# Optimization experiments

Hardware: AMD Instinct MI355X
Metric: run time of the kernel (lower is better)

## Reference

```python
import jax, jax.numpy as jnp
import numpy as np


def _dct2(x):
    """DCT-II over last dim, scipy norm=None scaling (matches the torch rfft trick:
    X_k = 2 * sum_n x_n cos(pi*k*(2n+1)/(2N))). Expressed as one batched matmul."""
    N = x.shape[-1]
    n = jnp.arange(N, dtype=x.dtype)
    k = jnp.arange(N, dtype=x.dtype)
    # D[k, n] = 2*cos(pi*k*(2n+1)/(2N))
    D = 2.0 * jnp.cos((np.pi / (2.0 * N)) * k[:, None] * (2.0 * n[None, :] + 1.0))
    return jnp.einsum('kn,bcn->bck', D, x)


def setup_inputs() -> dict:
    key = jax.random.key(0)
    k0, k1, k2 = jax.random.split(key, 3)
    b, c, l = 32, 512, 1024
    x = jax.random.normal(k0, (b, c, l), dtype=jnp.float32)
    # 1x1 Conv1d weights (kernel_size=1, bias=False) stored as [out, in]
    w1 = jax.random.normal(k1, (2 * c, c), dtype=jnp.float32) / np.float32(np.sqrt(c))
    w2 = jax.random.normal(k2, (c, 2 * c), dtype=jnp.float32) / np.float32(np.sqrt(2 * c))
    ln_w = jnp.ones((l,), dtype=jnp.float32)
    ln_b = jnp.zeros((l,), dtype=jnp.float32)
    return {"x": x, "w1": w1, "w2": w2, "ln_w": ln_w, "ln_b": ln_b}


def reference(x, w1, w2, ln_w, ln_b):
    eps = 1e-6
    freq = _dct2(x)                                   # [b, c, l]
    mu = jnp.mean(freq, axis=-1, keepdims=True)
    var = jnp.var(freq, axis=-1, keepdims=True)       # biased, like nn.LayerNorm
    h = (freq - mu) * jax.lax.rsqrt(var + eps) * ln_w + ln_b
    # fc: Conv1d(c->2c, k=1) -> Dropout(eval: identity) -> ReLU -> Conv1d(2c->c) -> Sigmoid
    h = jax.nn.relu(jnp.einsum('oi,bil->bol', w1, h))  # [b, 2c, l]
    gate = jax.nn.sigmoid(jnp.einsum('oi,bil->bol', w2, h))  # [b, c, l]
    return x * gate
```

## Files before the change

### kernel.cpp

```cpp
#include <hip/hip_runtime.h>
#include <hip/hip_bf16.h>
#include <math.h>

typedef short short8 __attribute__((ext_vector_type(8)));
typedef short short4v __attribute__((ext_vector_type(4)));
typedef float f32x4 __attribute__((ext_vector_type(4)));

__device__ __forceinline__ short f2bf(float f) {
  union { float f; unsigned u; } v; v.f = f;
  unsigned r = v.u + 0x7FFFu + ((v.u >> 16) & 1u);
  return (short)(r >> 16);
}
__device__ __forceinline__ float bf2f(short s) {
  union { unsigned u; float f; } v; v.u = ((unsigned)(unsigned short)s) << 16;
  return v.f;
}

__global__ __launch_bounds__(256) void cast_kernel(const float* __restrict__ in,
                                                   short* __restrict__ out, int n4) {
  int i = blockIdx.x * blockDim.x + threadIdx.x;
  if (i < n4) {
    float4 v = ((const float4*)in)[i];
    short4v o;
    o.x = f2bf(v.x); o.y = f2bf(v.y); o.z = f2bf(v.z); o.w = f2bf(v.w);
    ((short4v*)out)[i] = o;
  }
}

__global__ __launch_bounds__(256) void prep_eo(const float* __restrict__ x,
                                               short* __restrict__ eo) {
  int t = blockIdx.x * 256 + threadIdx.x;
  int bc = t >> 7, n0 = (t & 127) * 4;
  const float* xr = x + (size_t)bc * 1024;
  float4 f = *(const float4*)(xr + n0);
  float4 r = *(const float4*)(xr + 1020 - n0);
  short4v ef, of;
  ef.x = f2bf(f.x + r.w); ef.y = f2bf(f.y + r.z); ef.z = f2bf(f.z + r.y); ef.w = f2bf(f.w + r.x);
  of.x = f2bf(f.x - r.w); of.y = f2bf(f.y - r.z); of.z = f2bf(f.z - r.y); of.w = f2bf(f.w - r.x);
  *(short4v*)&eo[(size_t)bc * 512 + n0] = ef;
  *(short4v*)&eo[8388608 + (size_t)bc * 512 + n0] = of;
}

__global__ __launch_bounds__(256) void build_Deo(short* __restrict__ D) {
  int t = blockIdx.x * 256 + threadIdx.x;
  int parity = t >> 18, rem = t & 262143;
  int k2 = rem >> 9, n = rem & 511;
  const float s = 1.5339807878856412e-03f;
  float arg = (s * (float)(2 * k2 + parity)) * (float)(2 * n + 1);
  D[t] = f2bf(2.0f * cosf(arg));
}

__global__ __launch_bounds__(256) void ln_stats(const float2* __restrict__ partial,
                                                float2* __restrict__ musd) {
  int n = blockIdx.x * 256 + threadIdx.x;
  float S = 0.f, Q = 0.f;
#pragma unroll
  for (int r = 0; r < 8; ++r) {
    float2 p = partial[(size_t)r * 16384 + n];
    S += p.x; Q += p.y;
  }
  float mu  = S * (1.f / 1024.f);
  float var = Q * (1.f / 1024.f) - mu * mu;
  float2 o; o.x = mu; o.y = rsqrtf(var + 1e-6f);
  musd[n] = o;
}

__global__ __launch_bounds__(256) void ln_apply(short* __restrict__ freqT,
                                                const float2* __restrict__ musd,
                                                const float* __restrict__ lnw,
                                                const float* __restrict__ lnb) {
  int t = blockIdx.x * 256 + threadIdx.x;
  int c8 = t & 63;
  int k  = (t >> 6) & 1023;
  int b  = t >> 16;
  size_t idx = ((size_t)b << 19) + (size_t)k * 512 + (size_t)c8 * 8;
  short8 v = *(const short8*)&freqT[idx];
  float w  = lnw[k];
  float bb = lnb[k];
  const float2* ms = &musd[b * 512 + c8 * 8];
  short8 o;
#pragma unroll
  for (int j = 0; j < 8; ++j) {
    float f = bf2f(v[j]);
    float2 m = ms[j];
    o[j] = f2bf((f - m.x) * m.y * w + bb);
  }
  *(short8*)&freqT[idx] = o;
}

template<int EPI>
__global__ __launch_bounds__(256, 2) void gemm128(
    const short* __restrict__ A, const short* __restrict__ B,
    void* __restrict__ Cout, const float* __restrict__ X,
    float2* __restrict__ P, int K, int NT, long strideA, long strideB)
{
  __shared__ short As[2][8192];
  __shared__ short Bs[2][8192];
  const int tid = threadIdx.x;
  const int l   = tid & 63;
  const int w   = tid >> 6;
  const int wm  = w >> 1;
  const int wc  = w & 1;
  const int l7  = l & 7;
  const int lr  = l & 15;
  const int lhi = l >> 4;

  const int nwg = gridDim.x, q = nwg >> 3, orig = blockIdx.x;
  const int wgid = (orig & 7) * q + (orig >> 3);
  int bx, by, bz;
  if (EPI == 0)      { bx = wgid & 3; bz = (wgid >> 2) & 1; by = wgid >> 3; }
  else if (EPI == 1) { by = wgid & 7; bx = (wgid >> 3) & 7; bz = wgid >> 6; }
  else               { bx = wgid & 3; by = (wgid >> 2) & 7; bz = wgid >> 5; }

  const long row0 = (long)bx * 128, col0 = (long)by * 128;
  const short* Ab = A + (size_t)bz * strideA + (size_t)row0 * K;
  const short* Bb = B + (size_t)bz * strideB + (size_t)col0 * K;

  const int rowb  = tid >> 3;
  const int colel = ((tid & 7) ^ ((tid >> 3) & 7)) * 8;
  const int abase = (wm * 64 + lr) * 64;
  const int bbase = (wc * 64 + lr) * 64;
  const int s0 = ((lhi    ) ^ l7) * 8;
  const int s1 = ((lhi + 4) ^ l7) * 8;

  f32x4 acc[4][4];
#pragma unroll
  for (int i = 0; i < 4; ++i)
#pragma unroll
    for (int j = 0; j < 4; ++j) acc[i][j] = (f32x4){0.f, 0.f, 0.f, 0.f};

#define GLL(SRC, DST) __builtin_amdgcn_global_load_lds(                      \
      (const __attribute__((address_space(1))) void*)(SRC),                  \
      (__attribute__((address_space(3))) void*)(DST), 16, 0, 0)

#define STAGE(KT, D) do {                                                    \
    const size_t ko_ = (size_t)(KT) * 64 + colel;                            \
    _Pragma("unroll")                                                        \
    for (int r_ = 0; r_ < 4; ++r_)                                           \
      GLL(Ab + (size_t)(r_ * 32 + rowb) * K + ko_,                           \
          &As[D][(r_ * 32 + rowb) * 64 + (tid & 7) * 8]);                    \
    _Pragma("unroll")                                                        \
    for (int r_ = 0; r_ < 4; ++r_)                                           \
      GLL(Bb + (size_t)(r_ * 32 + rowb) * K + ko_,                           \
          &Bs[D][(r_ * 32 + rowb) * 64 + (tid & 7) * 8]);                    \
  } while (0)

#define LD8(PTR, OFF) (*(const short8*)&(PTR)[OFF])
#define MFMA(AV, BV, C) __builtin_amdgcn_mfma_f32_16x16x32_bf16(AV, BV, C, 0, 0, 0)
#define SBAR __builtin_amdgcn_s_barrier()
#define SCHB __builtin_amdgcn_sched_barrier(0)

#define MFMA16(A0, A1, A2, A3, B0, B1, B2, B3)                               \
    __builtin_amdgcn_s_setprio(1);                                           \
    acc[0][0]=MFMA(A0,B0,acc[0][0]); acc[0][1]=MFMA(A0,B1,acc[0][1]);        \
    acc[0][2]=MFMA(A0,B2,acc[0][2]); acc[0][3]=MFMA(A0,B3,acc[0][3]);        \
    acc[1][0]=MFMA(A1,B0,acc[1][0]); acc[1][1]=MFMA(A1,B1,acc[1][1]);        \
    acc[1][2]=MFMA(A1,B2,acc[1][2]); acc[1][3]=MFMA(A1,B3,acc[1][3]);        \
    acc[2][0]=MFMA(A2,B0,acc[2][0]); acc[2][1]=MFMA(A2,B1,acc[2][1]);        \
    acc[2][2]=MFMA(A2,B2,acc[2][2]); acc[2][3]=MFMA(A2,B3,acc[2][3]);        \
    acc[3][0]=MFMA(A3,B0,acc[3][0]); acc[3][1]=MFMA(A3,B1,acc[3][1]);        \
    acc[3][2]=MFMA(A3,B2,acc[3][2]); acc[3][3]=MFMA(A3,B3,acc[3][3]);        \
    __builtin_amdgcn_s_setprio(0);

  STAGE(0, 0);
  STAGE(1, 1);

  int cur = 0;
  for (int kt = 0; kt < NT; ++kt) {
    if (kt + 1 < NT) { asm volatile("s_waitcnt vmcnt(8)" ::: "memory"); }
    else             { asm volatile("s_waitcnt vmcnt(0)" ::: "memory"); }
    SCHB; SBAR;
    const short* Ad = As[cur];
    const short* Bd = Bs[cur];
    short8 a00, a01, a02, a03, b00, b01, b02, b03;
    short8 a10, a11, a12, a13, b10, b11, b12, b13;
    a00 = LD8(Ad, abase + 0 * 1024 + s0);
    a01 = LD8(Ad, abase + 1 * 1024 + s0);
    a02 = LD8(Ad, abase + 2 * 1024 + s0);
    a03 = LD8(Ad, abase + 3 * 1024 + s0);
    b00 = LD8(Bd, bbase + 0 * 1024 + s0);
    b01 = LD8(Bd, bbase + 1 * 1024 + s0);
    b02 = LD8(Bd, bbase + 2 * 1024 + s0);
    b03 = LD8(Bd, bbase + 3 * 1024 + s0);
    a10 = LD8(Ad, abase + 0 * 1024 + s1);
    a11 = LD8(Ad, abase + 1 * 1024 + s1);
    a12 = LD8(Ad, abase + 2 * 1024 + s1);
    a13 = LD8(Ad, abase + 3 * 1024 + s1);
    b10 = LD8(Bd, bbase + 0 * 1024 + s1);
    b11 = LD8(Bd, bbase + 1 * 1024 + s1);
    b12 = LD8(Bd, bbase + 2 * 1024 + s1);
    b13 = LD8(Bd, bbase + 3 * 1024 + s1);
    SCHB;
    asm volatile("s_waitcnt lgkmcnt(8)" ::: "memory");
    SCHB;
    MFMA16(a00, a01, a02, a03, b00, b01, b02, b03)
    SCHB;
    asm volatile("s_waitcnt lgkmcnt(0)" ::: "memory");
    SCHB; SBAR;
    if (kt + 2 < NT) STAGE(kt + 2, cur);
    SCHB;
    MFMA16(a10, a11, a12, a13, b10, b11, b12, b13)
    SCHB;
    cur ^= 1;
  }

  float sv[4], qv[4];
#pragma unroll
  for (int ni = 0; ni < 4; ++ni) { sv[ni] = 0.f; qv[ni] = 0.f; }

#pragma unroll
  for (int mi = 0; mi < 4; ++mi) {
#pragma unroll
    for (int ni = 0; ni < 4; ++ni) {
#pragma unroll
      for (int j = 0; j < 4; ++j) {
        int r  = (int)row0 + wm * 64 + mi * 16 + lhi * 4 + j;
        int cc = (int)col0 + wc * 64 + ni * 16 + lr;
        float v = acc[mi][ni][j];
        if (EPI == 0) {
          sv[ni] += v; qv[ni] += v * v;
          int rr = r * 2 + bz;
          ((short*)Cout)[((size_t)(cc >> 9) << 19) + (size_t)rr * 512 + (cc & 511)] = f2bf(v);
        } else if (EPI == 1) {
          ((short*)Cout)[(size_t)bz * 1048576 + (size_t)r * 1024 + cc] = f2bf(v > 0.f ? v : 0.f);
        } else {
          size_t idx = (size_t)bz * 524288 + (size_t)r * 1024 + cc;
          float g = 1.f / (1.f + __expf(-v));
          ((float*)Cout)[idx] = X[idx] * g;
        }
      }
    }
  }

  if (EPI == 0) {
    __syncthreads();
    float* redS = (float*)&As[0][0];
    float* redQ = redS + 1024;
    const int contrib = wm * 4 + lhi;
#pragma unroll
    for (int ni = 0; ni < 4; ++ni) {
      int ccl = wc * 64 + ni * 16 + lr;
      redS[ccl * 8 + contrib] = sv[ni];
      redQ[ccl * 8 + contrib] = qv[ni];
    }
    __syncthreads();
    if (tid < 128) {
      float S = 0.f, Q = 0.f;
#pragma unroll
      for (int i = 0; i < 8; ++i) { S += redS[tid * 8 + i]; Q += redQ[tid * 8 + i]; }
      float2 o; o.x = S; o.y = Q;
      P[(size_t)(bz * 4 + bx) * 16384 + col0 + tid] = o;
    }
  }
#undef MFMA16
#undef MFMA
#undef LD8
#undef STAGE
#undef GLL
#undef SBAR
#undef SCHB
}

extern "C" void kernel_launch(void* const* d_in, const int* in_sizes, int n_in,
                              void* d_out, int out_size, void* d_ws, size_t ws_size,
                              hipStream_t stream) {
  const float* x    = (const float*)d_in[0];
  const float* w1   = (const float*)d_in[1];
  const float* w2   = (const float*)d_in[2];
  const float* ln_w = (const float*)d_in[3];
  const float* ln_b = (const float*)d_in[4];
  float* out = (float*)d_out;

  char* ws = (char*)d_ws;
  short* Deo    = (short*)(ws);
  short* w1_bf  = (short*)(ws + 1048576);
  short* w2_bf  = (short*)(ws + 2097152);
  short* freqT  = (short*)(ws + 3145728);
  short* z1t    = (short*)(ws + 36700160);
  short* eo     = z1t;
  float2* part  = (float2*)(ws + 103809024);
  float2* musd  = (float2*)(ws + 104857600);

  prep_eo<<<dim3(8192), dim3(256), 0, stream>>>(x, eo);
  cast_kernel<<<dim3(512), dim3(256), 0, stream>>>(w1, w1_bf, 524288 / 4);
  cast_kernel<<<dim3(512), dim3(256), 0, stream>>>(w2, w2_bf, 524288 / 4);
  build_Deo<<<dim3(2048), dim3(256), 0, stream>>>(Deo);

  gemm128<0><<<dim3(1024), dim3(256), 0, stream>>>(
      Deo, eo, (void*)freqT, nullptr, part, 512, 8, 262144, 8388608);

  ln_stats<<<dim3(64), dim3(256), 0, stream>>>(part, musd);

  ln_apply<<<dim3(8192), dim3(256), 0, stream>>>(freqT, musd, ln_w, ln_b);

  gemm128<1><<<dim3(2048), dim3(256), 0, stream>>>(
      freqT, w1_bf, (void*)z1t, nullptr, nullptr, 512, 8, 524288, 0);

  gemm128<2><<<dim3(1024), dim3(256), 0, stream>>>(
      w2_bf, z1t, (void*)out, x, nullptr, 1024, 16, 0, 1048576);
}
```

Measured before the change: 160.5 us.

## Fuse LayerNorm apply into first FC GEMM via operand prologue and epilogue

Removes the separate ln_apply pass over freqT and instead normalizes the A operand (subtract mean, scale by rstd) in registers while staging it into LDS inside a new gemm2ln kernel. The per-k ln weight and bias are applied in the epilogue, using precomputed row sums of w1 computed during the w1 cast. This saves a full read-modify-write of the bf16 frequency tensor and one kernel launch. In exchange, A loads now go through registers instead of direct-to-LDS loads, which adds VALU work and register pressure inside the GEMM main loop.

```diff
diff --git a/kernel.cpp b/kernel.cpp
--- a/kernel.cpp
+++ b/kernel.cpp
@@ -14,6 +14,11 @@
 __device__ __forceinline__ float bf2f(short s) {
   union { unsigned u; float f; } v; v.u = ((unsigned)(unsigned short)s) << 16;
   return v.f;
+}
+__device__ __forceinline__ unsigned cvtpk(float lo, float hi) {
+  unsigned r;
+  asm("v_cvt_pk_bf16_f32 %0, %1, %2" : "=v"(r) : "v"(lo), "v"(hi));
+  return r;
 }
 
 __global__ __launch_bounds__(256) void cast_kernel(const float* __restrict__ in,
@@ -24,6 +29,30 @@
     short4v o;
     o.x = f2bf(v.x); o.y = f2bf(v.y); o.z = f2bf(v.z); o.w = f2bf(v.w);
     ((short4v*)out)[i] = o;
+  }
+}
+
+__global__ __launch_bounds__(256) void w1_prep(const float* __restrict__ w1,
+                                               short* __restrict__ w1_bf,
+                                               float* __restrict__ w1s) {
+  int t = blockIdx.x * 256 + threadIdx.x;
+  int o = t >> 2, qt = t & 3;
+  const float* src = w1 + (size_t)o * 512 + qt * 128;
+  short* dst = w1_bf + (size_t)o * 512 + qt * 128;
+  float s = 0.f;
+#pragma unroll
+  for (int i = 0; i < 128; i += 4) {
+    float4 v = *(const float4*)(src + i);
+    s += v.x + v.y + v.z + v.w;
+    short4v ov; ov.x = f2bf(v.x); ov.y = f2bf(v.y); ov.z = f2bf(v.z); ov.w = f2bf(v.w);
+    *(short4v*)(dst + i) = ov;
+  }
+  __shared__ float red[256];
+  red[threadIdx.x] = s;
+  __syncthreads();
+  if (qt == 0) {
+    int tx = threadIdx.x;
+    w1s[o] = red[tx] + red[tx + 1] + red[tx + 2] + red[tx + 3];
   }
 }
 
@@ -63,29 +92,6 @@
   float var = Q * (1.f / 1024.f) - mu * mu;
   float2 o; o.x = mu; o.y = rsqrtf(var + 1e-6f);
   musd[n] = o;
-}
-
-__global__ __launch_bounds__(256) void ln_apply(short* __restrict__ freqT,
-                                                const float2* __restrict__ musd,
-                                                const float* __restrict__ lnw,
-                                                const float* __restrict__ lnb) {
-  int t = blockIdx.x * 256 + threadIdx.x;
-  int c8 = t & 63;
-  int k  = (t >> 6) & 1023;
-  int b  = t >> 16;
-  size_t idx = ((size_t)b << 19) + (size_t)k * 512 + (size_t)c8 * 8;
-  short8 v = *(const short8*)&freqT[idx];
-  float w  = lnw[k];
-  float bb = lnb[k];
-  const float2* ms = &musd[b * 512 + c8 * 8];
-  short8 o;
-#pragma unroll
-  for (int j = 0; j < 8; ++j) {
-    float f = bf2f(v[j]);
-    float2 m = ms[j];
-    o[j] = f2bf((f - m.x) * m.y * w + bb);
-  }
-  *(short8*)&freqT[idx] = o;
 }
 
 template<int EPI>
@@ -109,7 +115,6 @@
   const int wgid = (orig & 7) * q + (orig >> 3);
   int bx, by, bz;
   if (EPI == 0)      { bx = wgid & 3; bz = (wgid >> 2) & 1; by = wgid >> 3; }
-  else if (EPI == 1) { by = wgid & 7; bx = (wgid >> 3) & 7; bz = wgid >> 6; }
   else               { bx = wgid & 3; by = (wgid >> 2) & 7; bz = wgid >> 5; }
 
   const long row0 = (long)bx * 128, col0 = (long)by * 128;
@@ -221,8 +226,6 @@
           sv[ni] += v; qv[ni] += v * v;
           int rr = r * 2 + bz;
           ((short*)Cout)[((size_t)(cc >> 9) << 19) + (size_t)rr * 512 + (cc & 511)] = f2bf(v);
-        } else if (EPI == 1) {
-          ((short*)Cout)[(size_t)bz * 1048576 + (size_t)r * 1024 + cc] = f2bf(v > 0.f ? v : 0.f);
         } else {
           size_t idx = (size_t)bz * 524288 + (size_t)r * 1024 + cc;
           float g = 1.f / (1.f + __expf(-v));
@@ -253,10 +256,196 @@
     }
   }
 #undef MFMA16
+#undef STAGE
+}
+
+__global__ __launch_bounds__(256, 2) void gemm2ln(
+    const short* __restrict__ A, const short* __restrict__ B,
+    short* __restrict__ Cout, const float2* __restrict__ musd,
+    const float* __restrict__ lnw, const float* __restrict__ lnb,
+    const float* __restrict__ w1s)
+{
+  const int K = 512, NT = 8;
+  __shared__ short As[2][8192];
+  __shared__ short Bs[2][8192];
+  const int tid = threadIdx.x;
+  const int l   = tid & 63;
+  const int w   = tid >> 6;
+  const int wm  = w >> 1;
+  const int wc  = w & 1;
+  const int l7  = l & 7;
+  const int lr  = l & 15;
+  const int lhi = l >> 4;
+
+  const int nwg = gridDim.x, q = nwg >> 3, orig = blockIdx.x;
+  const int wgid = (orig & 7) * q + (orig >> 3);
+  const int by = wgid & 7, bx = (wgid >> 3) & 7, bz = wgid >> 6;
+
+  const long row0 = (long)bx * 128, col0 = (long)by * 128;
+  const short* Ab = A + (size_t)bz * 524288 + (size_t)row0 * K;
+  const short* Bb = B + (size_t)col0 * K;
+  const float2* msb = musd + bz * 512;
+
+  const int rowb  = tid >> 3;
+  const int slot  = tid & 7;
+  const int colel = (slot ^ (rowb & 7)) * 8;
+  const int abase = (wm * 64 + lr) * 64;
+  const int bbase = (wc * 64 + lr) * 64;
+  const int s0 = ((lhi    ) ^ l7) * 8;
+  const int s1 = ((lhi + 4) ^ l7) * 8;
+
+  f32x4 acc[4][4];
+#pragma unroll
+  for (int i = 0; i < 4; ++i)
+#pragma unroll
+    for (int j = 0; j < 4; ++j) acc[i][j] = (f32x4){0.f, 0.f, 0.f, 0.f};
+
+#define SBAR __builtin_amdgcn_s_barrier()
+#define SCHB __builtin_amdgcn_sched_barrier(0)
+#define LD8(PTR, OFF) (*(const short8*)&(PTR)[OFF])
+#define MFMA(AV, BV, C) __builtin_amdgcn_mfma_f32_16x16x32_bf16(AV, BV, C, 0, 0, 0)
+#define GLLB(SRC, DST) __builtin_amdgcn_global_load_lds(                     \
+      (const __attribute__((address_space(1))) void*)(SRC),                  \
+      (__attribute__((address_space(3))) void*)(DST), 16, 0, 0)
+
+  short8 ar0, ar1, ar2, ar3;
+  float4 m01, m23, m45, m67;
+
+#define ISSUE(KT, D) do {                                                    \
+    const size_t ko_ = (size_t)(KT) * 64 + colel;                            \
+    _Pragma("unroll")                                                        \
+    for (int r_ = 0; r_ < 4; ++r_)                                           \
+      GLLB(Bb + (size_t)(r_ * 32 + rowb) * K + ko_,                          \
+           &Bs[D][(r_ * 32 + rowb) * 64 + slot * 8]);                        \
+    ar0 = LD8(Ab, (size_t)(0 * 32 + rowb) * K + ko_);                        \
+    ar1 = LD8(Ab, (size_t)(1 * 32 + rowb) * K + ko_);                        \
+    ar2 = LD8(Ab, (size_t)(2 * 32 + rowb) * K + ko_);                        \
+    ar3 = LD8(Ab, (size_t)(3 * 32 + rowb) * K + ko_);                        \
+    const float* mp_ = (const float*)&msb[(KT) * 64 + colel];                \
+    m01 = *(const float4*)(mp_ + 0);                                         \
+    m23 = *(const float4*)(mp_ + 4);                                         \
+    m45 = *(const float4*)(mp_ + 8);                                         \
+    m67 = *(const float4*)(mp_ + 12);                                        \
+  } while (0)
+
+#define XFORM_ONE(AV, DROW, D) do {                                          \
+    unsigned u0_ = cvtpk((bf2f(AV[0]) - m01.x) * m01.y,                      \
+                         (bf2f(AV[1]) - m01.z) * m01.w);                     \
+    unsigned u1_ = cvtpk((bf2f(AV[2]) - m23.x) * m23.y,                      \
+                         (bf2f(AV[3]) - m23.z) * m23.w);                     \
+    unsigned u2_ = cvtpk((bf2f(AV[4]) - m45.x) * m45.y,                      \
+                         (bf2f(AV[5]) - m45.z) * m45.w);                     \
+    unsigned u3_ = cvtpk((bf2f(AV[6]) - m67.x) * m67.y,                      \
+                         (bf2f(AV[7]) - m67.z) * m67.w);                     \
+    int4 wv_; wv_.x = (int)u0_; wv_.y = (int)u1_; wv_.z = (int)u2_; wv_.w = (int)u3_; \
+    *(int4*)&As[D][((DROW) * 32 + rowb) * 64 + slot * 8] = wv_;              \
+  } while (0)
+
+#define XFORM(D) do {                                                        \
+    XFORM_ONE(ar0, 0, D); XFORM_ONE(ar1, 1, D);                              \
+    XFORM_ONE(ar2, 2, D); XFORM_ONE(ar3, 3, D);                              \
+  } while (0)
+
+  ISSUE(0, 0);
+  asm volatile("s_waitcnt vmcnt(0)" ::: "memory");
+  SCHB;
+  XFORM(0);
+  ISSUE(1, 1);
+  asm volatile("s_waitcnt lgkmcnt(0)" ::: "memory");
+  SCHB;
+
+  int cur = 0;
+  for (int kt = 0; kt < NT; ++kt) {
+    SBAR;
+    const short* Ad = As[cur];
+    const short* Bd = Bs[cur];
+    short8 a00, a01, a02, a03, b00, b01, b02, b03;
+    short8 a10, a11, a12, a13, b10, b11, b12, b13;
+    a00 = LD8(Ad, abase + 0 * 1024 + s0);
+    a01 = LD8(Ad, abase + 1 * 1024 + s0);
+    a02 = LD8(Ad, abase + 2 * 1024 + s0);
+    a03 = LD8(Ad, abase + 3 * 1024 + s0);
+    b00 = LD8(Bd, bbase + 0 * 1024 + s0);
+    b01 = LD8(Bd, bbase + 1 * 1024 + s0);
+    b02 = LD8(Bd, bbase + 2 * 1024 + s0);
+    b03 = LD8(Bd, bbase + 3 * 1024 + s0);
+    a10 = LD8(Ad, abase + 0 * 1024 + s1);
+    a11 = LD8(Ad, abase + 1 * 1024 + s1);
+    a12 = LD8(Ad, abase + 2 * 1024 + s1);
+    a13 = LD8(Ad, abase + 3 * 1024 + s1);
+    b10 = LD8(Bd, bbase + 0 * 1024 + s1);
+    b11 = LD8(Bd, bbase + 1 * 1024 + s1);
+    b12 = LD8(Bd, bbase + 2 * 1024 + s1);
+    b13 = LD8(Bd, bbase + 3 * 1024 + s1);
+    SCHB;
+    if (kt + 1 < NT) {
+      asm volatile("s_waitcnt vmcnt(0)" ::: "memory");
+      SCHB;
+      XFORM(cur ^ 1);
+      SCHB;
+      asm volatile("s_waitcnt lgkmcnt(12)" ::: "memory");
+    } else {
+      asm volatile("s_waitcnt lgkmcnt(8)" ::: "memory");
+    }
+    SCHB;
+    __builtin_amdgcn_s_setprio(1);
+    acc[0][0]=MFMA(a00,b00,acc[0][0]); acc[0][1]=MFMA(a00,b01,acc[0][1]);
+    acc[0][2]=MFMA(a00,b02,acc[0][2]); acc[0][3]=MFMA(a00,b03,acc[0][3]);
+    acc[1][0]=MFMA(a01,b00,acc[1][0]); acc[1][1]=MFMA(a01,b01,acc[1][1]);
+    acc[1][2]=MFMA(a01,b02,acc[1][2]); acc[1][3]=MFMA(a01,b03,acc[1][3]);
+    acc[2][0]=MFMA(a02,b00,acc[2][0]); acc[2][1]=MFMA(a02,b01,acc[2][1]);
+    acc[2][2]=MFMA(a02,b02,acc[2][2]); acc[2][3]=MFMA(a02,b03,acc[2][3]);
+    acc[3][0]=MFMA(a03,b00,acc[3][0]); acc[3][1]=MFMA(a03,b01,acc[3][1]);
+    acc[3][2]=MFMA(a03,b02,acc[3][2]); acc[3][3]=MFMA(a03,b03,acc[3][3]);
+    __builtin_amdgcn_s_setprio(0);
+    SCHB;
+    if (kt + 1 < NT) { asm volatile("s_waitcnt lgkmcnt(4)" ::: "memory"); }
+    else             { asm volatile("s_waitcnt lgkmcnt(0)" ::: "memory"); }
+    SCHB; SBAR;
+    if (kt + 2 < NT) ISSUE(kt + 2, cur);
+    SCHB;
+    __builtin_amdgcn_s_setprio(1);
+    acc[0][0]=MFMA(a10,b10,acc[0][0]); acc[0][1]=MFMA(a10,b11,acc[0][1]);
+    acc[0][2]=MFMA(a10,b12,acc[0][2]); acc[0][3]=MFMA(a10,b13,acc[0][3]);
+    acc[1][0]=MFMA(a11,b10,acc[1][0]); acc[1][1]=MFMA(a11,b11,acc[1][1]);
+    acc[1][2]=MFMA(a11,b12,acc[1][2]); acc[1][3]=MFMA(a11,b13,acc[1][3]);
+    acc[2][0]=MFMA(a12,b10,acc[2][0]); acc[2][1]=MFMA(a12,b11,acc[2][1]);
+    acc[2][2]=MFMA(a12,b12,acc[2][2]); acc[2][3]=MFMA(a12,b13,acc[2][3]);
+    acc[3][0]=MFMA(a13,b10,acc[3][0]); acc[3][1]=MFMA(a13,b11,acc[3][1]);
+    acc[3][2]=MFMA(a13,b12,acc[3][2]); acc[3][3]=MFMA(a13,b13,acc[3][3]);
+    __builtin_amdgcn_s_setprio(0);
+    SCHB;
+    asm volatile("s_waitcnt lgkmcnt(0)" ::: "memory");
+    SCHB;
+    cur ^= 1;
+  }
+
+  const int rb = (int)row0 + wm * 64 + lhi * 4;
+  const int cb = (int)col0 + wc * 64 + lr;
+#pragma unroll
+  for (int mi = 0; mi < 4; ++mi) {
+    float4 wv4 = *(const float4*)&lnw[rb + mi * 16];
+    float4 bv4 = *(const float4*)&lnb[rb + mi * 16];
+#pragma unroll
+    for (int ni = 0; ni < 4; ++ni) {
+      int cc = cb + ni * 16;
+      float ws = w1s[cc];
+#pragma unroll
+      for (int j = 0; j < 4; ++j) {
+        int r = rb + mi * 16 + j;
+        float lw = (j == 0) ? wv4.x : (j == 1) ? wv4.y : (j == 2) ? wv4.z : wv4.w;
+        float lb = (j == 0) ? bv4.x : (j == 1) ? bv4.y : (j == 2) ? bv4.z : bv4.w;
+        float v = lw * acc[mi][ni][j] + lb * ws;
+        Cout[(size_t)bz * 1048576 + (size_t)r * 1024 + cc] = f2bf(v > 0.f ? v : 0.f);
+      }
+    }
+  }
+#undef XFORM
+#undef XFORM_ONE
+#undef ISSUE
+#undef GLLB
 #undef MFMA
 #undef LD8
-#undef STAGE
-#undef GLL
 #undef SBAR
 #undef SCHB
 }
@@ -280,9 +469,10 @@
   short* eo     = z1t;
   float2* part  = (float2*)(ws + 103809024);
   float2* musd  = (float2*)(ws + 104857600);
+  float*  w1s   = (float*)(ws + 104988672);
 
   prep_eo<<<dim3(8192), dim3(256), 0, stream>>>(x, eo);
-  cast_kernel<<<dim3(512), dim3(256), 0, stream>>>(w1, w1_bf, 524288 / 4);
+  w1_prep<<<dim3(16), dim3(256), 0, stream>>>(w1, w1_bf, w1s);
   cast_kernel<<<dim3(512), dim3(256), 0, stream>>>(w2, w2_bf, 524288 / 4);
   build_Deo<<<dim3(2048), dim3(256), 0, stream>>>(Deo);
 
@@ -291,10 +481,8 @@
 
   ln_stats<<<dim3(64), dim3(256), 0, stream>>>(part, musd);
 
-  ln_apply<<<dim3(8192), dim3(256), 0, stream>>>(freqT, musd, ln_w, ln_b);
-
-  gemm128<1><<<dim3(2048), dim3(256), 0, stream>>>(
-      freqT, w1_bf, (void*)z1t, nullptr, nullptr, 512, 8, 524288, 0);
+  gemm2ln<<<dim3(2048), dim3(256), 0, stream>>>(
+      freqT, w1_bf, z1t, musd, ln_w, ln_b, w1s);
 
   gemm128<2><<<dim3(1024), dim3(256), 0, stream>>>(
       w2_bf, z1t, (void*)out, x, nullptr, 1024, 16, 0, 1048576);
```

After: 172.6 us. +7.5%, slower.

## Load weight fragments directly from global memory, staging only streaming operand in LDS

Applied to the files above, without the earlier changes.

The GEMM kernel now stages only the streaming (activation) operand through LDS and reads the weight/DCT operand fragments straight from global memory into registers each k-step. This halves LDS usage so occupancy is raised to 3 blocks per CU, and it cuts LDS traffic and global-to-LDS copies. In exchange, each wave issues uncoalesced 16-byte global loads per fragment, relying on L2/L1 caching of the small, heavily shared weights. The wait and barrier schedule is reworked around the new load mix.

```diff
diff --git a/kernel.cpp b/kernel.cpp
--- a/kernel.cpp
+++ b/kernel.cpp
@@ -89,13 +89,12 @@
 }
 
 template<int EPI>
-__global__ __launch_bounds__(256, 2) void gemm128(
-    const short* __restrict__ A, const short* __restrict__ B,
+__global__ __launch_bounds__(256, 3) void gemmW(
+    const short* __restrict__ Wp, const short* __restrict__ Sp,
     void* __restrict__ Cout, const float* __restrict__ X,
-    float2* __restrict__ P, int K, int NT, long strideA, long strideB)
+    float2* __restrict__ P, int K, int NT, long strideW, long strideS)
 {
-  __shared__ short As[2][8192];
-  __shared__ short Bs[2][8192];
+  __shared__ short Ss[2][8192];
   const int tid = threadIdx.x;
   const int l   = tid & 63;
   const int w   = tid >> 6;
@@ -113,13 +112,18 @@
   else               { bx = wgid & 3; by = (wgid >> 2) & 7; bz = wgid >> 5; }
 
   const long row0 = (long)bx * 128, col0 = (long)by * 128;
-  const short* Ab = A + (size_t)bz * strideA + (size_t)row0 * K;
-  const short* Bb = B + (size_t)bz * strideB + (size_t)col0 * K;
+  const int wS = (EPI == 1) ? wm : wc;
+  const int wW = (EPI == 1) ? wc : wm;
+  const short* Wb = Wp + (size_t)bz * strideW
+                  + (size_t)((EPI == 1) ? col0 : row0) * K
+                  + (size_t)(wW * 64 + lr) * K;
+  const short* Sb = Sp + (size_t)bz * strideS
+                  + (size_t)((EPI == 1) ? row0 : col0) * K;
 
   const int rowb  = tid >> 3;
-  const int colel = ((tid & 7) ^ ((tid >> 3) & 7)) * 8;
-  const int abase = (wm * 64 + lr) * 64;
-  const int bbase = (wc * 64 + lr) * 64;
+  const int slot  = tid & 7;
+  const int colel = (slot ^ (rowb & 7)) * 8;
+  const int sbase = (wS * 64 + lr) * 64;
   const int s0 = ((lhi    ) ^ l7) * 8;
   const int s1 = ((lhi + 4) ^ l7) * 8;
 
@@ -133,16 +137,12 @@
       (const __attribute__((address_space(1))) void*)(SRC),                  \
       (__attribute__((address_space(3))) void*)(DST), 16, 0, 0)
 
-#define STAGE(KT, D) do {                                                    \
+#define STAGE_S(KT, D) do {                                                  \
     const size_t ko_ = (size_t)(KT) * 64 + colel;                            \
     _Pragma("unroll")                                                        \
     for (int r_ = 0; r_ < 4; ++r_)                                           \
-      GLL(Ab + (size_t)(r_ * 32 + rowb) * K + ko_,                           \
-          &As[D][(r_ * 32 + rowb) * 64 + (tid & 7) * 8]);                    \
-    _Pragma("unroll")                                                        \
-    for (int r_ = 0; r_ < 4; ++r_)                                           \
-      GLL(Bb + (size_t)(r_ * 32 + rowb) * K + ko_,                           \
-          &Bs[D][(r_ * 32 + rowb) * 64 + (tid & 7) * 8]);                    \
+      GLL(Sb + (size_t)(r_ * 32 + rowb) * K + ko_,                           \
+          &Ss[D][(r_ * 32 + rowb) * 64 + slot * 8]);                         \
   } while (0)
 
 #define LD8(PTR, OFF) (*(const short8*)&(PTR)[OFF])
@@ -150,56 +150,46 @@
 #define SBAR __builtin_amdgcn_s_barrier()
 #define SCHB __builtin_amdgcn_sched_barrier(0)
 
-#define MFMA16(A0, A1, A2, A3, B0, B1, B2, B3)                               \
+#define QUADK(WF, SF)                                                        \
     __builtin_amdgcn_s_setprio(1);                                           \
-    acc[0][0]=MFMA(A0,B0,acc[0][0]); acc[0][1]=MFMA(A0,B1,acc[0][1]);        \
-    acc[0][2]=MFMA(A0,B2,acc[0][2]); acc[0][3]=MFMA(A0,B3,acc[0][3]);        \
-    acc[1][0]=MFMA(A1,B0,acc[1][0]); acc[1][1]=MFMA(A1,B1,acc[1][1]);        \
-    acc[1][2]=MFMA(A1,B2,acc[1][2]); acc[1][3]=MFMA(A1,B3,acc[1][3]);        \
-    acc[2][0]=MFMA(A2,B0,acc[2][0]); acc[2][1]=MFMA(A2,B1,acc[2][1]);        \
-    acc[2][2]=MFMA(A2,B2,acc[2][2]); acc[2][3]=MFMA(A2,B3,acc[2][3]);        \
-    acc[3][0]=MFMA(A3,B0,acc[3][0]); acc[3][1]=MFMA(A3,B1,acc[3][1]);        \
-    acc[3][2]=MFMA(A3,B2,acc[3][2]); acc[3][3]=MFMA(A3,B3,acc[3][3]);        \
+    _Pragma("unroll")                                                        \
+    for (int i_ = 0; i_ < 4; ++i_)                                           \
+    _Pragma("unroll")                                                        \
+      for (int j_ = 0; j_ < 4; ++j_)                                         \
+        acc[i_][j_] = (EPI == 1) ? MFMA(SF[i_], WF[j_], acc[i_][j_])         \
+                                 : MFMA(WF[i_], SF[j_], acc[i_][j_]);        \
     __builtin_amdgcn_s_setprio(0);
 
-  STAGE(0, 0);
-  STAGE(1, 1);
-
+  STAGE_S(0, 0);
+  STAGE_S(1, 1);
+
+  short8 wf0[4], wf1[4], sf0[4], sf1[4];
   int cur = 0;
   for (int kt = 0; kt < NT; ++kt) {
-    if (kt + 1 < NT) { asm volatile("s_waitcnt vmcnt(8)" ::: "memory"); }
-    else             { asm volatile("s_waitcnt vmcnt(0)" ::: "memory"); }
+    if (kt == 0) { asm volatile("s_waitcnt vmcnt(4)" ::: "memory"); }
     SCHB; SBAR;
-    const short* Ad = As[cur];
-    const short* Bd = Bs[cur];
-    short8 a00, a01, a02, a03, b00, b01, b02, b03;
-    short8 a10, a11, a12, a13, b10, b11, b12, b13;
-    a00 = LD8(Ad, abase + 0 * 1024 + s0);
-    a01 = LD8(Ad, abase + 1 * 1024 + s0);
-    a02 = LD8(Ad, abase + 2 * 1024 + s0);
-    a03 = LD8(Ad, abase + 3 * 1024 + s0);
-    b00 = LD8(Bd, bbase + 0 * 1024 + s0);
-    b01 = LD8(Bd, bbase + 1 * 1024 + s0);
-    b02 = LD8(Bd, bbase + 2 * 1024 + s0);
-    b03 = LD8(Bd, bbase + 3 * 1024 + s0);
-    a10 = LD8(Ad, abase + 0 * 1024 + s1);
-    a11 = LD8(Ad, abase + 1 * 1024 + s1);
-    a12 = LD8(Ad, abase + 2 * 1024 + s1);
-    a13 = LD8(Ad, abase + 3 * 1024 + s1);
-    b10 = LD8(Bd, bbase + 0 * 1024 + s1);
-    b11 = LD8(Bd, bbase + 1 * 1024 + s1);
-    b12 = LD8(Bd, bbase + 2 * 1024 + s1);
-    b13 = LD8(Bd, bbase + 3 * 1024 + s1);
-    SCHB;
-    asm volatile("s_waitcnt lgkmcnt(8)" ::: "memory");
-    SCHB;
-    MFMA16(a00, a01, a02, a03, b00, b01, b02, b03)
-    SCHB;
-    asm volatile("s_waitcnt lgkmcnt(0)" ::: "memory");
+    const short* Sd = Ss[cur];
+    const size_t wko = (size_t)kt * 64 + lhi * 8;
+#pragma unroll
+    for (int i = 0; i < 4; ++i) {
+      wf0[i] = LD8(Wb, (size_t)(i * 16) * K + wko);
+      wf1[i] = LD8(Wb, (size_t)(i * 16) * K + wko + 32);
+    }
+    SCHB;
+#pragma unroll
+    for (int i = 0; i < 4; ++i) sf0[i] = LD8(Sd, sbase + i * 1024 + s0);
+#pragma unroll
+    for (int i = 0; i < 4; ++i) sf1[i] = LD8(Sd, sbase + i * 1024 + s1);
+    SCHB;
+    asm volatile("s_waitcnt lgkmcnt(4)" ::: "memory");
+    SCHB;
+    QUADK(wf0, sf0)
+    SCHB;
+    asm volatile("s_waitcnt vmcnt(0) lgkmcnt(0)" ::: "memory");
     SCHB; SBAR;
-    if (kt + 2 < NT) STAGE(kt + 2, cur);
-    SCHB;
-    MFMA16(a10, a11, a12, a13, b10, b11, b12, b13)
+    QUADK(wf1, sf1)
+    SCHB;
+    if (kt + 2 < NT) STAGE_S(kt + 2, cur);
     SCHB;
     cur ^= 1;
   }
@@ -234,7 +224,7 @@
 
   if (EPI == 0) {
     __syncthreads();
-    float* redS = (float*)&As[0][0];
+    float* redS = (float*)&Ss[0][0];
     float* redQ = redS + 1024;
     const int contrib = wm * 4 + lhi;
 #pragma unroll
@@ -252,10 +242,10 @@
       P[(size_t)(bz * 4 + bx) * 16384 + col0 + tid] = o;
     }
   }
-#undef MFMA16
+#undef QUADK
 #undef MFMA
 #undef LD8
-#undef STAGE
+#undef STAGE_S
 #undef GLL
 #undef SBAR
 #undef SCHB
@@ -286,16 +276,16 @@
   cast_kernel<<<dim3(512), dim3(256), 0, stream>>>(w2, w2_bf, 524288 / 4);
   build_Deo<<<dim3(2048), dim3(256), 0, stream>>>(Deo);
 
-  gemm128<0><<<dim3(1024), dim3(256), 0, stream>>>(
+  gemmW<0><<<dim3(1024), dim3(256), 0, stream>>>(
       Deo, eo, (void*)freqT, nullptr, part, 512, 8, 262144, 8388608);
 
   ln_stats<<<dim3(64), dim3(256), 0, stream>>>(part, musd);
 
   ln_apply<<<dim3(8192), dim3(256), 0, stream>>>(freqT, musd, ln_w, ln_b);
 
-  gemm128<1><<<dim3(2048), dim3(256), 0, stream>>>(
-      freqT, w1_bf, (void*)z1t, nullptr, nullptr, 512, 8, 524288, 0);
-
-  gemm128<2><<<dim3(1024), dim3(256), 0, stream>>>(
+  gemmW<1><<<dim3(2048), dim3(256), 0, stream>>>(
+      w1_bf, freqT, (void*)z1t, nullptr, nullptr, 512, 8, 0, 524288);
+
+  gemmW<2><<<dim3(1024), dim3(256), 0, stream>>>(
       w2_bf, z1t, (void*)out, x, nullptr, 1024, 16, 0, 1048576);
 }
```

New measurement: 238.2 us. 48.4% more time.

## Use dedicated 256x128 tile GEMM with BK=32 for the DCT stage

Applied to the files above, without the earlier changes.

Adds a new gemmF kernel for the DCT GEMM that uses a 256-row by 128-column output tile with a K step of 32, an 8x4 MFMA accumulator per wave, a new LDS swizzle and setprio around the MFMA bursts. Larger M tiles halve the grid and the number of partial LN stat rows, so ln_stats now reduces 4 partials instead of 8. The LN-stat epilogue is removed from gemm128. The aim is more reuse of the B operand per loaded tile and less epilogue and stat-reduction work. In exchange the kernel holds more accumulator registers, which may hurt occupancy, and the shorter K step doubles the number of loop iterations and barriers.

```diff
diff --git a/kernel.cpp b/kernel.cpp
--- a/kernel.cpp
+++ b/kernel.cpp
@@ -55,7 +55,7 @@
   int n = blockIdx.x * 256 + threadIdx.x;
   float S = 0.f, Q = 0.f;
 #pragma unroll
-  for (int r = 0; r < 8; ++r) {
+  for (int r = 0; r < 4; ++r) {
     float2 p = partial[(size_t)r * 16384 + n];
     S += p.x; Q += p.y;
   }
@@ -89,10 +89,166 @@
 }
 
 template<int EPI>
+__global__ __launch_bounds__(256, 2) void gemmF(
+    const short* __restrict__ A, const short* __restrict__ B,
+    void* __restrict__ Cout, const float* __restrict__ X,
+    float2* __restrict__ P, int K, int NT, long strideA, long strideB)
+{
+  __shared__ short As[2][8192];
+  __shared__ short Bs[2][4096];
+  const int tid = threadIdx.x;
+  const int l   = tid & 63;
+  const int w   = tid >> 6;
+  const int wm  = w >> 1;
+  const int wc  = w & 1;
+  const int lr  = l & 15;
+  const int lhi = l >> 4;
+
+  const int nwg = gridDim.x, q = nwg >> 3, orig = blockIdx.x;
+  const int wgid = (orig & 7) * q + (orig >> 3);
+  int bx, by, bz;
+  bx = wgid & 1; bz = (wgid >> 1) & 1; by = wgid >> 2;
+
+  const long row0 = (long)bx * 256, col0 = (long)by * 128;
+  const short* Ab = A + (size_t)bz * strideA + (size_t)row0 * K;
+  const short* Bb = B + (size_t)bz * strideB + (size_t)col0 * K;
+
+  const int sx    = (lhi ^ ((lr >> 1) & 3)) * 8;
+  const int abase = (wm * 128 + lr) * 32;
+  const int bbase = (wc * 64  + lr) * 32;
+
+  f32x4 acc[8][4];
+#pragma unroll
+  for (int i = 0; i < 8; ++i)
+#pragma unroll
+    for (int j = 0; j < 4; ++j) acc[i][j] = (f32x4){0.f, 0.f, 0.f, 0.f};
+
+#define GLL(SRC, DST) __builtin_amdgcn_global_load_lds(                      \
+      (const __attribute__((address_space(1))) void*)(SRC),                  \
+      (__attribute__((address_space(3))) void*)(DST), 16, 0, 0)
+
+#define STAGE(KT, D) do {                                                    \
+    const size_t kb_ = (size_t)(KT) * 32;                                    \
+    _Pragma("unroll")                                                        \
+    for (int r_ = 0; r_ < 4; ++r_) {                                         \
+      int c_ = r_ * 256 + tid; int row_ = c_ >> 2; int sl_ = c_ & 3;         \
+      int sc_ = (sl_ ^ ((row_ >> 1) & 3)) * 8;                               \
+      GLL(Ab + (size_t)row_ * K + kb_ + sc_, &As[D][row_ * 32 + sl_ * 8]);   \
+    }                                                                        \
+    _Pragma("unroll")                                                        \
+    for (int r_ = 0; r_ < 2; ++r_) {                                         \
+      int c_ = r_ * 256 + tid; int row_ = c_ >> 2; int sl_ = c_ & 3;         \
+      int sc_ = (sl_ ^ ((row_ >> 1) & 3)) * 8;                               \
+      GLL(Bb + (size_t)row_ * K + kb_ + sc_, &Bs[D][row_ * 32 + sl_ * 8]);   \
+    }                                                                        \
+  } while (0)
+
+#define LD8(PTR, OFF) (*(const short8*)&(PTR)[OFF])
+#define MFMA(AV, BV, C) __builtin_amdgcn_mfma_f32_16x16x32_bf16(AV, BV, C, 0, 0, 0)
+#define SBAR __builtin_amdgcn_s_barrier()
+#define SCHB __builtin_amdgcn_sched_barrier(0)
+
+#define MROW(MI, AV)                                                         \
+    acc[MI][0] = MFMA(AV, b0, acc[MI][0]);                                   \
+    acc[MI][1] = MFMA(AV, b1, acc[MI][1]);                                   \
+    acc[MI][2] = MFMA(AV, b2, acc[MI][2]);                                   \
+    acc[MI][3] = MFMA(AV, b3, acc[MI][3]);
+
+  STAGE(0, 0);
+  STAGE(1, 1);
+
+  int cur = 0;
+  for (int kt = 0; kt < NT; ++kt) {
+    if (kt + 1 < NT) { asm volatile("s_waitcnt vmcnt(6)" ::: "memory"); }
+    else             { asm volatile("s_waitcnt vmcnt(0)" ::: "memory"); }
+    SCHB; SBAR;
+    const short* Ad = As[cur];
+    const short* Bd = Bs[cur];
+    short8 a0, a1, a2, a3, a4, a5, a6, a7, b0, b1, b2, b3;
+    a0 = LD8(Ad, abase + 0 * 512 + sx);
+    a1 = LD8(Ad, abase + 1 * 512 + sx);
+    b0 = LD8(Bd, bbase + 0 * 512 + sx);
+    b1 = LD8(Bd, bbase + 1 * 512 + sx);
+    b2 = LD8(Bd, bbase + 2 * 512 + sx);
+    b3 = LD8(Bd, bbase + 3 * 512 + sx);
+    a2 = LD8(Ad, abase + 2 * 512 + sx);
+    a3 = LD8(Ad, abase + 3 * 512 + sx);
+    a4 = LD8(Ad, abase + 4 * 512 + sx);
+    a5 = LD8(Ad, abase + 5 * 512 + sx);
+    a6 = LD8(Ad, abase + 6 * 512 + sx);
+    a7 = LD8(Ad, abase + 7 * 512 + sx);
+    SCHB;
+    asm volatile("s_waitcnt lgkmcnt(6)" ::: "memory");
+    SCHB;
+    __builtin_amdgcn_s_setprio(1);
+    MROW(0, a0) MROW(1, a1)
+    __builtin_amdgcn_s_setprio(0);
+    SCHB;
+    asm volatile("s_waitcnt lgkmcnt(0)" ::: "memory");
+    SCHB; SBAR;
+    if (kt + 2 < NT) STAGE(kt + 2, cur);
+    SCHB;
+    __builtin_amdgcn_s_setprio(1);
+    MROW(2, a2) MROW(3, a3) MROW(4, a4) MROW(5, a5) MROW(6, a6) MROW(7, a7)
+    __builtin_amdgcn_s_setprio(0);
+    SCHB;
+    cur ^= 1;
+  }
+
+  float sv[4], qv[4];
+#pragma unroll
+  for (int ni = 0; ni < 4; ++ni) { sv[ni] = 0.f; qv[ni] = 0.f; }
+
+#pragma unroll
+  for (int mi = 0; mi < 8; ++mi) {
+#pragma unroll
+    for (int ni = 0; ni < 4; ++ni) {
+#pragma unroll
+      for (int j = 0; j < 4; ++j) {
+        int r  = (int)row0 + wm * 128 + mi * 16 + lhi * 4 + j;
+        int cc = (int)col0 + wc * 64 + ni * 16 + lr;
+        float v = acc[mi][ni][j];
+        sv[ni] += v; qv[ni] += v * v;
+        int rr = r * 2 + bz;
+        ((short*)Cout)[((size_t)(cc >> 9) << 19) + (size_t)rr * 512 + (cc & 511)] = f2bf(v);
+      }
+    }
+  }
+
+  {
+    __syncthreads();
+    float* redS = (float*)&As[0][0];
+    float* redQ = redS + 1024;
+    const int contrib = wm * 4 + lhi;
+#pragma unroll
+    for (int ni = 0; ni < 4; ++ni) {
+      int ccl = wc * 64 + ni * 16 + lr;
+      redS[ccl * 8 + contrib] = sv[ni];
+      redQ[ccl * 8 + contrib] = qv[ni];
+    }
+    __syncthreads();
+    if (tid < 128) {
+      float S = 0.f, Q = 0.f;
+#pragma unroll
+      for (int i = 0; i < 8; ++i) { S += redS[tid * 8 + i]; Q += redQ[tid * 8 + i]; }
+      float2 o; o.x = S; o.y = Q;
+      P[(size_t)(bz * 2 + bx) * 16384 + col0 + tid] = o;
+    }
+  }
+#undef MROW
+#undef MFMA
+#undef LD8
+#undef STAGE
+#undef GLL
+#undef SBAR
+#undef SCHB
+}
+
+template<int EPI>
 __global__ __launch_bounds__(256, 2) void gemm128(
     const short* __restrict__ A, const short* __restrict__ B,
     void* __restrict__ Cout, const float* __restrict__ X,
-    float2* __restrict__ P, int K, int NT, long strideA, long strideB)
+    int K, int NT, long strideA, long strideB)
 {
   __shared__ short As[2][8192];
   __shared__ short Bs[2][8192];
@@ -108,9 +264,8 @@
   const int nwg = gridDim.x, q = nwg >> 3, orig = blockIdx.x;
   const int wgid = (orig & 7) * q + (orig >> 3);
   int bx, by, bz;
-  if (EPI == 0)      { bx = wgid & 3; bz = (wgid >> 2) & 1; by = wgid >> 3; }
-  else if (EPI == 1) { by = wgid & 7; bx = (wgid >> 3) & 7; bz = wgid >> 6; }
-  else               { bx = wgid & 3; by = (wgid >> 2) & 7; bz = wgid >> 5; }
+  if (EPI == 1) { by = wgid & 7; bx = (wgid >> 3) & 7; bz = wgid >> 6; }
+  else          { bx = wgid & 3; by = (wgid >> 2) & 7; bz = wgid >> 5; }
 
   const long row0 = (long)bx * 128, col0 = (long)by * 128;
   const short* Ab = A + (size_t)bz * strideA + (size_t)row0 * K;
@@ -204,10 +359,6 @@
     cur ^= 1;
   }
 
-  float sv[4], qv[4];
-#pragma unroll
-  for (int ni = 0; ni < 4; ++ni) { sv[ni] = 0.f; qv[ni] = 0.f; }
-
 #pragma unroll
   for (int mi = 0; mi < 4; ++mi) {
 #pragma unroll
@@ -217,11 +368,7 @@
         int r  = (int)row0 + wm * 64 + mi * 16 + lhi * 4 + j;
         int cc = (int)col0 + wc * 64 + ni * 16 + lr;
         float v = acc[mi][ni][j];
-        if (EPI == 0) {
-          sv[ni] += v; qv[ni] += v * v;
-          int rr = r * 2 + bz;
-          ((short*)Cout)[((size_t)(cc >> 9) << 19) + (size_t)rr * 512 + (cc & 511)] = f2bf(v);
-        } else if (EPI == 1) {
+        if (EPI == 1) {
           ((short*)Cout)[(size_t)bz * 1048576 + (size_t)r * 1024 + cc] = f2bf(v > 0.f ? v : 0.f);
         } else {
           size_t idx = (size_t)bz * 524288 + (size_t)r * 1024 + cc;
@@ -229,27 +376,6 @@
           ((float*)Cout)[idx] = X[idx] * g;
         }
       }
-    }
-  }
-
-  if (EPI == 0) {
-    __syncthreads();
-    float* redS = (float*)&As[0][0];
-    float* redQ = redS + 1024;
-    const int contrib = wm * 4 + lhi;
-#pragma unroll
-    for (int ni = 0; ni < 4; ++ni) {
-      int ccl = wc * 64 + ni * 16 + lr;
-      redS[ccl * 8 + contrib] = sv[ni];
-      redQ[ccl * 8 + contrib] = qv[ni];
-    }
-    __syncthreads();
-    if (tid < 128) {
-      float S = 0.f, Q = 0.f;
-#pragma unroll
-      for (int i = 0; i < 8; ++i) { S += redS[tid * 8 + i]; Q += redQ[tid * 8 + i]; }
-      float2 o; o.x = S; o.y = Q;
-      P[(size_t)(bz * 4 + bx) * 16384 + col0 + tid] = o;
     }
   }
 #undef MFMA16
@@ -286,16 +412,16 @@
   cast_kernel<<<dim3(512), dim3(256), 0, stream>>>(w2, w2_bf, 524288 / 4);
   build_Deo<<<dim3(2048), dim3(256), 0, stream>>>(Deo);
 
-  gemm128<0><<<dim3(1024), dim3(256), 0, stream>>>(
-      Deo, eo, (void*)freqT, nullptr, part, 512, 8, 262144, 8388608);
+  gemmF<0><<<dim3(512), dim3(256), 0, stream>>>(
+      Deo, eo, (void*)freqT, nullptr, part, 512, 16, 262144, 8388608);
 
   ln_stats<<<dim3(64), dim3(256), 0, stream>>>(part, musd);
 
   ln_apply<<<dim3(8192), dim3(256), 0, stream>>>(freqT, musd, ln_w, ln_b);
 
   gemm128<1><<<dim3(2048), dim3(256), 0, stream>>>(
-      freqT, w1_bf, (void*)z1t, nullptr, nullptr, 512, 8, 524288, 0);
+      freqT, w1_bf, (void*)z1t, nullptr, 512, 8, 524288, 0);
 
   gemm128<2><<<dim3(1024), dim3(256), 0, stream>>>(
-      w2_bf, z1t, (void*)out, x, nullptr, 1024, 16, 0, 1048576);
-}
+      w2_bf, z1t, (void*)out, x, 1024, 16, 0, 1048576);
+}
```

New measurement: 156.7 us. -2.4%, faster.
